# Kernel optimization log

Hardware: AMD Instinct MI355X
Metric: run time of the kernel (lower is better)

## Reference

```python
import jax, jax.numpy as jnp
import numpy as np

B, S, D, H = 4, 2048, 1024, 16
DK = D // H
THETA = 10000.0


def setup_inputs() -> dict:
    key = jax.random.key(0)
    ks = jax.random.split(key, 5)
    std = (1.0 / D) ** 0.5
    return {
        "x": jax.random.normal(ks[0], (B, S, D), dtype=jnp.float32),
        "q_proj": jax.random.normal(ks[1], (D, D), dtype=jnp.float32) * std,
        "k_proj": jax.random.normal(ks[2], (D, D), dtype=jnp.float32) * std,
        "v_proj": jax.random.normal(ks[3], (D, D), dtype=jnp.float32) * std,
        "o_proj": jax.random.normal(ks[4], (D, D), dtype=jnp.float32) * std,
        "token_positions": jnp.broadcast_to(jnp.arange(S, dtype=jnp.int32), (B, S)),
    }


def _apply_rope(t, cos, sin):
    # t: (B,H,S,DK); cos/sin: (B,1,S,DK//2). Interleaved even/odd rotation.
    even = t[..., 0::2]
    odd = t[..., 1::2]
    r_even = even * cos - odd * sin
    r_odd = even * sin + odd * cos
    return jnp.stack([r_even, r_odd], axis=-1).reshape(t.shape)


def reference(x, q_proj, k_proj, v_proj, o_proj, token_positions):
    b, s, d = x.shape
    # QKV projections: weights stored (out, in) -> x @ W^T
    q = (x @ q_proj.T).reshape(b, s, H, DK).transpose(0, 2, 1, 3)  # (B,H,S,DK)
    k = (x @ k_proj.T).reshape(b, s, H, DK).transpose(0, 2, 1, 3)
    v = (x @ v_proj.T).reshape(b, s, H, DK).transpose(0, 2, 1, 3)

    # RoPE angles from token positions
    inv_freq = 1.0 / (THETA ** (jnp.arange(0, DK, 2, dtype=jnp.float32) / DK))  # (DK/2,)
    ang = token_positions.astype(jnp.float32)[..., None] * inv_freq  # (B,S,DK/2)
    cos = jnp.cos(ang)[:, None, :, :]  # (B,1,S,DK/2)
    sin = jnp.sin(ang)[:, None, :, :]
    q = _apply_rope(q, cos, sin)
    k = _apply_rope(k, cos, sin)

    # Full causal attention with explicit score matrix (faithful to source)
    scores = jnp.einsum("bhqd,bhkd->bhqk", q, k) / (DK ** 0.5)
    causal = jnp.tril(jnp.ones((s, s), dtype=bool))
    scores = jnp.where(causal, scores, -jnp.inf)
    attn = jax.nn.softmax(scores, axis=-1)
    out = jnp.einsum("bhqk,bhkd->bhqd", attn, v)  # (B,H,S,DK)
    out = out.transpose(0, 2, 1, 3).reshape(b, s, d)  # (B,S,D)
    # o_proj stored (d_out, d_model): out @ o_proj^T
    return out @ o_proj.T
```

## Files before the change

### kernel.cpp

```cpp
#include <hip/hip_runtime.h>
#include <hip/hip_bf16.h>

using bf16x8 = __attribute__((ext_vector_type(8))) short;
using f32x4  = __attribute__((ext_vector_type(4))) float;

#define MFMA_BF16(a, b, c) __builtin_amdgcn_mfma_f32_16x16x32_bf16((a), (b), (c), 0, 0, 0)

__device__ __forceinline__ unsigned short f2bf(float x) {
  union { float f; unsigned int u; } v; v.f = x;
  unsigned int r = v.u + 0x7fffu + ((v.u >> 16) & 1u);
  return (unsigned short)(r >> 16);
}

__device__ __forceinline__ unsigned int cvtpk(float a, float b) {
  __hip_bfloat162 h = __float22bfloat162_rn(make_float2(a, b));
  unsigned int u; __builtin_memcpy(&u, &h, 4); return u;
}

__device__ __forceinline__ unsigned int pack_trunc(float a, float b) {
  unsigned int ua, ub;
  __builtin_memcpy(&ua, &a, 4);
  __builtin_memcpy(&ub, &b, 4);
  return (ua >> 16) | (ub & 0xFFFF0000u);
}

__device__ __forceinline__ float fast_exp2(float x) {
#if __has_builtin(__builtin_amdgcn_exp2f)
  return __builtin_amdgcn_exp2f(x);
#else
  return exp2f(x);
#endif
}

__device__ __forceinline__ void gload16(const void* g, void* l) {
  __builtin_amdgcn_global_load_lds(
      (const __attribute__((address_space(1))) unsigned int*)g,
      (__attribute__((address_space(3))) unsigned int*)l, 16, 0, 0);
}

__device__ __forceinline__ void wait_and_barrier() {
  asm volatile("s_waitcnt vmcnt(0)" ::: "memory");
  __builtin_amdgcn_sched_barrier(0);
  __builtin_amdgcn_s_barrier();
  __builtin_amdgcn_sched_barrier(0);
}

__global__ __launch_bounds__(256) void cvt_all(const float* __restrict__ x,
                                               const float* __restrict__ qw,
                                               const float* __restrict__ kw,
                                               const float* __restrict__ vw,
                                               const float* __restrict__ ow,
                                               unsigned short* __restrict__ out) {
  const int bid = blockIdx.x;
  int seg, loc;
  if (bid < 8192) { seg = 0; loc = bid; }
  else { seg = 1 + ((bid - 8192) >> 10); loc = (bid - 8192) & 1023; }
  const float* srcs[5] = {x, qw, kw, vw, ow};
  const float* in = srcs[seg];
  const size_t obase = (seg == 0) ? 0 : ((size_t)8192 + (size_t)(seg - 1) * 1024) * 1024;
  const int i = loc * 1024 + threadIdx.x * 4;
  float4 f = *(const float4*)(in + i);
  ushort4 o;
  o.x = f2bf(f.x); o.y = f2bf(f.y); o.z = f2bf(f.z); o.w = f2bf(f.w);
  *(ushort4*)(out + obase + i) = o;
}

__global__ __launch_bounds__(256) void rope_tab_k(const int* __restrict__ pos,
                                                  float2* __restrict__ tab) {
  const int row = blockIdx.x * 8 + (threadIdx.x >> 5);
  const int i = threadIdx.x & 31;
  const float p = (float)pos[row];
  const float invf = exp2f((float)(2 * i) * (-13.287712379549609f / 64.0f));
  float sn, cs;
  sincosf(p * invf, &sn, &cs);
  tab[(size_t)row * 32 + i] = make_float2(cs, sn);
}

template <int MODE>
__global__ __launch_bounds__(256) void gemm_bt(const unsigned short* __restrict__ A,
                                               const unsigned short* __restrict__ Bw,
                                               void* __restrict__ outp,
                                               const float2* __restrict__ tab,
                                               float oscale) {
  constexpr int K = 1024;
  __shared__ __align__(16) unsigned short smem[12288];
  const int tid  = threadIdx.x;
  const int lane = tid & 63, wave = tid >> 6;
  const int wr = wave >> 1, wc = wave & 1;
  const int bid = blockIdx.x + (blockIdx.y << 3);
  const int xcd = bid & 7;
  const int t6  = bid >> 3;
  const int bn0 = (t6 & 7) * 128;
  const int bm0 = (((t6 >> 3) << 3) + xcd) * 64;
  const int lrow = lane & 15, hi = lane >> 4, lko = hi * 8;
  const int srow = tid >> 2, scol = (tid & 3) * 8;
  const unsigned short* gA = A + (size_t)(bm0 + srow) * K + scol;
  const unsigned short* gB = Bw + (size_t)(bn0 + srow) * K + scol;
  const f32x4 z = {0.f, 0.f, 0.f, 0.f};
  f32x4 acc[2][4];
#pragma unroll
  for (int i = 0; i < 2; ++i)
#pragma unroll
    for (int j = 0; j < 4; ++j) acc[i][j] = z;

  auto stage = [&](int k0, int c) {
    char* base = (char*)smem + c * 12288;
    gload16(gA + k0, base + wave * 1024);
    gload16(gB + k0, base + 4096 + wave * 1024);
    gload16(gB + k0 + (size_t)64 * K, base + 8192 + wave * 1024);
  };

  stage(0, 0);
  int cur = 0;
#pragma unroll 1
  for (int k0 = 0; k0 < K; k0 += 32) {
    wait_and_barrier();
    if (k0 + 32 < K) stage(k0 + 32, cur ^ 1);
    const int ub = cur * 6144;
    bf16x8 af[2], bfr[4];
#pragma unroll
    for (int mi = 0; mi < 2; ++mi)
      af[mi] = *(const bf16x8*)&smem[ub + (wr * 32 + mi * 16 + lrow) * 32 + lko];
#pragma unroll
    for (int ni = 0; ni < 4; ++ni)
      bfr[ni] = *(const bf16x8*)&smem[ub + 2048 + (wc * 64 + ni * 16 + lrow) * 32 + lko];
#pragma unroll
    for (int mi = 0; mi < 2; ++mi)
#pragma unroll
      for (int ni = 0; ni < 4; ++ni)
        acc[mi][ni] = MFMA_BF16(af[mi], bfr[ni], acc[mi][ni]);
    cur ^= 1;
  }

  if (MODE == 2) {
#pragma unroll
    for (int mi = 0; mi < 2; ++mi)
#pragma unroll
      for (int r = 0; r < 4; ++r) {
        const int row = bm0 + wr * 32 + mi * 16 + hi * 4 + r;
#pragma unroll
        for (int ni = 0; ni < 4; ++ni) {
          const int col = bn0 + wc * 64 + ni * 16 + lrow;
          ((float*)outp)[(size_t)row * 1024 + col] = acc[mi][ni][r];
        }
      }
    return;
  }

  const int h0 = bn0 >> 6;
  const int bb = bm0 >> 11, s0 = bm0 & 2047;
  unsigned short* dst = (unsigned short*)outp;
  __syncthreads();
  if (MODE == 0) {
#pragma unroll
    for (int mi = 0; mi < 2; ++mi)
#pragma unroll
      for (int ni = 0; ni < 4; ++ni) {
        const int col = wc * 64 + ni * 16 + lrow;
        const int d = col & 63;
#pragma unroll
        for (int r = 0; r < 4; ++r) {
          const int row = wr * 32 + mi * 16 + hi * 4 + r;
          const float2 t = tab[(size_t)(bm0 + row) * 32 + (d >> 1)];
          const float v = acc[mi][ni][r];
          const float other = __shfl_xor(v, 1);
          const float rv = (d & 1) ? (other * t.y + v * t.x) : (v * t.x - other * t.y);
          smem[row * 136 + col] = f2bf(rv * oscale);
        }
      }
    __syncthreads();
#pragma unroll
    for (int it = 0; it < 4; ++it) {
      const int c = it * 256 + tid;
      const int hl = c >> 9, rem = c & 511;
      const int sl = rem >> 3, ch = (rem & 7) * 8;
      const bf16x8 val = *(const bf16x8*)&smem[sl * 136 + hl * 64 + ch];
      *(bf16x8*)&dst[((size_t)(bb * 16 + h0 + hl) * 2048 + s0 + sl) * 64 + ch] = val;
    }
  } else {
#pragma unroll
    for (int mi = 0; mi < 2; ++mi)
#pragma unroll
      for (int ni = 0; ni < 4; ++ni) {
        const int col = wc * 64 + ni * 16 + lrow;
        ushort4 pk;
        pk.x = f2bf(acc[mi][ni][0]); pk.y = f2bf(acc[mi][ni][1]);
        pk.z = f2bf(acc[mi][ni][2]); pk.w = f2bf(acc[mi][ni][3]);
        *(ushort4*)&smem[col * 72 + wr * 32 + mi * 16 + hi * 4] = pk;
      }
    __syncthreads();
#pragma unroll
    for (int it = 0; it < 4; ++it) {
      const int c = it * 256 + tid;
      const int cl = c >> 3, sc = (c & 7) * 8;
      const bf16x8 val = *(const bf16x8*)&smem[cl * 72 + sc];
      *(bf16x8*)&dst[((size_t)(bb * 16 + h0 + (cl >> 6)) * 64 + (cl & 63)) * 2048 + s0 + sc] = val;
    }
  }
}

__global__ __launch_bounds__(256) void attn_fwd(const unsigned short* __restrict__ Q,
                                                const unsigned short* __restrict__ Kk,
                                                const unsigned short* __restrict__ Vt,
                                                unsigned short* __restrict__ O) {
  __shared__ __align__(16) unsigned short Ks[8192];
  __shared__ __align__(16) unsigned short Vs[8192];
  __shared__ __align__(16) unsigned short Plds[4][16][64];
  const int p = blockIdx.x;
  const int L = (p & 7) * 64 + (p >> 3);
  const int bh = L >> 3, pr = L & 7;
  const int tid = threadIdx.x;
  const int lane = tid & 63, wave = tid >> 6;
  const int lrow = lane & 15, hi = lane >> 4;
  const int l7 = lrow & 7;
  const unsigned short* Qb = Q + (size_t)bh * 2048 * 64;
  const unsigned short* Kb = Kk + (size_t)bh * 2048 * 64;
  const unsigned short* Vb = Vt + (size_t)bh * 64 * 2048;
  const int rK   = tid >> 3;
  const int colK = ((tid & 7) ^ ((tid >> 3) & 7)) * 8;
  const int rV   = tid >> 4;
  const int colV = ((tid & 8) | ((tid & 7) ^ ((tid >> 4) & 7))) * 8;
  const int b = bh >> 4, h = bh & 15;
  const f32x4 z = {0.f, 0.f, 0.f, 0.f};
  const short one = (short)0x3F80;
  const bf16x8 ones = {one, one, one, one, one, one, one, one};
  const int qrl = wave * 16 + lrow;

  auto stage128 = [&](int kv0) {
#pragma unroll
    for (int pass = 0; pass < 4; ++pass)
      gload16(Kb + (size_t)(kv0 + rK + 32 * pass) * 64 + colK,
              (char*)Ks + pass * 4096 + wave * 1024);
#pragma unroll
    for (int pass = 0; pass < 4; ++pass)
      gload16(Vb + (size_t)(rV + 16 * pass) * 2048 + kv0 + colV,
              (char*)Vs + pass * 4096 + wave * 1024);
  };

  for (int half = 0; half < 2; ++half) {
    const int qb = half ? (15 - pr) : pr;
    const int qga = qb * 128 + qrl;
    const int qgb = qga + 64;
    const bf16x8 qfa0 = *(const bf16x8*)(Qb + (size_t)qga * 64 + hi * 8);
    const bf16x8 qfa1 = *(const bf16x8*)(Qb + (size_t)qga * 64 + 32 + hi * 8);
    const bf16x8 qfb0 = *(const bf16x8*)(Qb + (size_t)qgb * 64 + hi * 8);
    const bf16x8 qfb1 = *(const bf16x8*)(Qb + (size_t)qgb * 64 + 32 + hi * 8);
    f32x4 acca[4] = {z, z, z, z}, accb[4] = {z, z, z, z};
    f32x4 acc_la = z, acc_lb = z;

    auto sm_pv = [&](f32x4* st, const bf16x8* vf, f32x4* acc, f32x4& acc_l,
                     bool dg) {
      if (dg) {
#pragma unroll
        for (int n = 0; n < 4; ++n)
#pragma unroll
          for (int r = 0; r < 4; ++r)
            if (n * 16 + hi * 4 + r > qrl) st[n][r] = -1e30f;
      }
      float pe[16];
#pragma unroll
      for (int n = 0; n < 4; ++n)
#pragma unroll
        for (int r = 0; r < 4; ++r) pe[n * 4 + r] = fast_exp2(st[n][r]);
#pragma unroll
      for (int n = 0; n < 4; ++n) {
        uint2 pk;
        pk.x = pack_trunc(pe[n * 4 + 0], pe[n * 4 + 1]);
        pk.y = pack_trunc(pe[n * 4 + 2], pe[n * 4 + 3]);
        const int eo = ((((n * 2 + (hi >> 1)) ^ l7) << 3) | ((hi & 1) << 2));
        *(uint2*)&Plds[wave][lrow][eo] = pk;
      }
      const bf16x8 pf0 = *(const bf16x8*)&Plds[wave][lrow][(hi ^ l7) << 3];
      const bf16x8 pf1 = *(const bf16x8*)&Plds[wave][lrow][((4 + hi) ^ l7) << 3];
      acc_l = MFMA_BF16(ones, pf0, acc_l);
      acc_l = MFMA_BF16(ones, pf1, acc_l);
#pragma unroll
      for (int dt = 0; dt < 4; ++dt) {
        acc[dt] = MFMA_BF16(vf[dt * 2], pf0, acc[dt]);
        acc[dt] = MFMA_BF16(vf[dt * 2 + 1], pf1, acc[dt]);
      }
    };

    auto process_half = [&](const char* Kbase, const char* Vbase,
                            bool doA, bool dgA, bool dgB) {
      bf16x8 kf[8];
#pragma unroll
      for (int n = 0; n < 4; ++n) {
        const int rk = n * 16 + lrow;
        kf[n * 2]     = *(const bf16x8*)(Kbase + rk * 128 + ((hi ^ l7) * 16));
        kf[n * 2 + 1] = *(const bf16x8*)(Kbase + rk * 128 + (((4 + hi) ^ l7) * 16));
      }
      f32x4 sta[4], stb[4];
      __builtin_amdgcn_s_setprio(1);
      if (doA) {
#pragma unroll
        for (int n = 0; n < 4; ++n) {
          sta[n] = MFMA_BF16(kf[n * 2], qfa0, z);
          sta[n] = MFMA_BF16(kf[n * 2 + 1], qfa1, sta[n]);
        }
      }
#pragma unroll
      for (int n = 0; n < 4; ++n) {
        stb[n] = MFMA_BF16(kf[n * 2], qfb0, z);
        stb[n] = MFMA_BF16(kf[n * 2 + 1], qfb1, stb[n]);
      }
      __builtin_amdgcn_s_setprio(0);
      bf16x8 vf[8];
#pragma unroll
      for (int dt = 0; dt < 4; ++dt) {
        const int rv = dt * 16 + lrow;
        vf[dt * 2]     = *(const bf16x8*)(Vbase + rv * 256 + ((hi ^ l7) * 16));
        vf[dt * 2 + 1] = *(const bf16x8*)(Vbase + rv * 256 + (((4 + hi) ^ l7) * 16));
      }
      if (doA) sm_pv(sta, vf, acca, acc_la, dgA);
      sm_pv(stb, vf, accb, acc_lb, dgB);
    };

#pragma unroll 1
    for (int f = 0; f <= qb; ++f) {
      __syncthreads();
      stage128(f * 128);
      __syncthreads();
      const bool dg = (f == qb);
      process_half((char*)Ks, (char*)Vs, true, dg, false);
      process_half((char*)Ks + 8192, (char*)Vs + 128, !dg, false, dg);
    }

    const float inva = 1.0f / acc_la[0];
    const float invb = 1.0f / acc_lb[0];
#pragma unroll
    for (int dt = 0; dt < 4; ++dt) {
      uint2 ov;
      ov.x = cvtpk(acca[dt][0] * inva, acca[dt][1] * inva);
      ov.y = cvtpk(acca[dt][2] * inva, acca[dt][3] * inva);
      *(uint2*)&O[((size_t)b * 2048 + qga) * 1024 + h * 64 + dt * 16 + hi * 4] = ov;
      uint2 ow2;
      ow2.x = cvtpk(accb[dt][0] * invb, accb[dt][1] * invb);
      ow2.y = cvtpk(accb[dt][2] * invb, accb[dt][3] * invb);
      *(uint2*)&O[((size_t)b * 2048 + qgb) * 1024 + h * 64 + dt * 16 + hi * 4] = ow2;
    }
  }
}

extern "C" void kernel_launch(void* const* d_in, const int* in_sizes, int n_in,
                              void* d_out, int out_size, void* d_ws, size_t ws_size,
                              hipStream_t stream) {
  const float* x  = (const float*)d_in[0];
  const float* qw = (const float*)d_in[1];
  const float* kw = (const float*)d_in[2];
  const float* vw = (const float*)d_in[3];
  const float* ow = (const float*)d_in[4];
  const int* pos  = (const int*)d_in[5];
  float* out = (float*)d_out;

  unsigned short* xb  = (unsigned short*)d_ws;
  unsigned short* qwb = xb  + (size_t)8192 * 1024;
  unsigned short* kwb = qwb + (size_t)1024 * 1024;
  unsigned short* vwb = kwb + (size_t)1024 * 1024;
  unsigned short* owb = vwb + (size_t)1024 * 1024;
  unsigned short* Qr  = owb + (size_t)1024 * 1024;
  unsigned short* Kr  = Qr  + (size_t)8192 * 1024;
  unsigned short* Vtr = Kr  + (size_t)8192 * 1024;
  unsigned short* AO  = Vtr + (size_t)8192 * 1024;
  float2* tab = (float2*)(AO + (size_t)8192 * 1024);

  cvt_all<<<12288, 256, 0, stream>>>(x, qw, kw, vw, ow, xb);
  rope_tab_k<<<1024, 256, 0, stream>>>(pos, tab);

  constexpr float SCALE = 0.18033688011112042f;
  dim3 gg(8, 128);
  gemm_bt<0><<<gg, 256, 0, stream>>>(xb, qwb, Qr,  tab, SCALE);
  gemm_bt<0><<<gg, 256, 0, stream>>>(xb, kwb, Kr,  tab, 1.0f);
  gemm_bt<1><<<gg, 256, 0, stream>>>(xb, vwb, Vtr, nullptr, 1.0f);
  attn_fwd<<<512, 256, 0, stream>>>(Qr, Kr, Vtr, AO);
  gemm_bt<2><<<gg, 256, 0, stream>>>(AO, owb, out, nullptr, 1.0f);
}
```

Measured before the change: 177.9 us.

## Use 128x128 GEMM tiles, merge QKV launches, fuse rope table into conversion

Enlarges the projection GEMM block tile from 64x128 to 128x128, giving each wave a 64x64 sub-tile. This raises MFMA work per LDS load and halves the grid. LDS reads get an XOR swizzle to avoid bank conflicts. The three Q/K/V GEMMs run as one launch using blockIdx.z, and the RoPE table computation is folded into the fp32-to-bf16 conversion kernel, which now converts 8 elements per thread. Launch count drops, at the cost of more accumulator registers, which may lower occupancy, and fewer blocks per GPU.

```diff
diff --git a/kernel.cpp b/kernel.cpp
--- a/kernel.cpp
+++ b/kernel.cpp
@@ -50,64 +50,75 @@
                                                const float* __restrict__ kw,
                                                const float* __restrict__ vw,
                                                const float* __restrict__ ow,
-                                               unsigned short* __restrict__ out) {
+                                               unsigned short* __restrict__ out,
+                                               const int* __restrict__ pos,
+                                               float2* __restrict__ tab) {
   const int bid = blockIdx.x;
+  if (bid >= 6144) {
+    const int row = (bid - 6144) * 8 + (threadIdx.x >> 5);
+    const int i = threadIdx.x & 31;
+    const float p = (float)pos[row];
+    const float invf = exp2f((float)(2 * i) * (-13.287712379549609f / 64.0f));
+    float sn, cs;
+    sincosf(p * invf, &sn, &cs);
+    tab[(size_t)row * 32 + i] = make_float2(cs, sn);
+    return;
+  }
   int seg, loc;
-  if (bid < 8192) { seg = 0; loc = bid; }
-  else { seg = 1 + ((bid - 8192) >> 10); loc = (bid - 8192) & 1023; }
+  if (bid < 4096) { seg = 0; loc = bid; }
+  else { seg = 1 + ((bid - 4096) >> 9); loc = (bid - 4096) & 511; }
   const float* srcs[5] = {x, qw, kw, vw, ow};
   const float* in = srcs[seg];
   const size_t obase = (seg == 0) ? 0 : ((size_t)8192 + (size_t)(seg - 1) * 1024) * 1024;
-  const int i = loc * 1024 + threadIdx.x * 4;
-  float4 f = *(const float4*)(in + i);
-  ushort4 o;
-  o.x = f2bf(f.x); o.y = f2bf(f.y); o.z = f2bf(f.z); o.w = f2bf(f.w);
-  *(ushort4*)(out + obase + i) = o;
-}
-
-__global__ __launch_bounds__(256) void rope_tab_k(const int* __restrict__ pos,
-                                                  float2* __restrict__ tab) {
-  const int row = blockIdx.x * 8 + (threadIdx.x >> 5);
-  const int i = threadIdx.x & 31;
-  const float p = (float)pos[row];
-  const float invf = exp2f((float)(2 * i) * (-13.287712379549609f / 64.0f));
-  float sn, cs;
-  sincosf(p * invf, &sn, &cs);
-  tab[(size_t)row * 32 + i] = make_float2(cs, sn);
+  const int i = loc * 2048 + threadIdx.x * 8;
+  float4 f0 = *(const float4*)(in + i);
+  float4 f1 = *(const float4*)(in + i + 4);
+  bf16x8 o;
+  o[0] = (short)f2bf(f0.x); o[1] = (short)f2bf(f0.y);
+  o[2] = (short)f2bf(f0.z); o[3] = (short)f2bf(f0.w);
+  o[4] = (short)f2bf(f1.x); o[5] = (short)f2bf(f1.y);
+  o[6] = (short)f2bf(f1.z); o[7] = (short)f2bf(f1.w);
+  *(bf16x8*)(out + obase + i) = o;
 }
 
 template <int MODE>
-__global__ __launch_bounds__(256) void gemm_bt(const unsigned short* __restrict__ A,
-                                               const unsigned short* __restrict__ Bw,
+__global__ __launch_bounds__(256) void gemm128(const unsigned short* __restrict__ A,
+                                               const unsigned short* __restrict__ W,
                                                void* __restrict__ outp,
-                                               const float2* __restrict__ tab,
-                                               float oscale) {
+                                               const float2* __restrict__ tab) {
   constexpr int K = 1024;
-  __shared__ __align__(16) unsigned short smem[12288];
+  constexpr float SCALE = 0.18033688011112042f;
+  constexpr int SMEM_ELEMS = (MODE == 0) ? 17408 : 16384;
+  __shared__ __align__(16) unsigned short smem[SMEM_ELEMS];
   const int tid  = threadIdx.x;
   const int lane = tid & 63, wave = tid >> 6;
   const int wr = wave >> 1, wc = wave & 1;
+  const int z = (MODE == 0) ? blockIdx.z : 0;
+  const unsigned short* Bw = W + (size_t)z * 1048576;
   const int bid = blockIdx.x + (blockIdx.y << 3);
   const int xcd = bid & 7;
   const int t6  = bid >> 3;
   const int bn0 = (t6 & 7) * 128;
-  const int bm0 = (((t6 >> 3) << 3) + xcd) * 64;
-  const int lrow = lane & 15, hi = lane >> 4, lko = hi * 8;
-  const int srow = tid >> 2, scol = (tid & 3) * 8;
+  const int bm0 = (((t6 >> 3) << 3) + xcd) * 128;
+  const int lrow = lane & 15, hi = lane >> 4;
+  const int srow = tid >> 2;
+  const int scol = ((tid & 3) ^ (srow & 3) ^ ((srow >> 2) & 3)) * 8;
   const unsigned short* gA = A + (size_t)(bm0 + srow) * K + scol;
   const unsigned short* gB = Bw + (size_t)(bn0 + srow) * K + scol;
-  const f32x4 z = {0.f, 0.f, 0.f, 0.f};
-  f32x4 acc[2][4];
-#pragma unroll
-  for (int i = 0; i < 2; ++i)
-#pragma unroll
-    for (int j = 0; j < 4; ++j) acc[i][j] = z;
+  const int sw2 = (lrow & 3) ^ ((lrow >> 2) & 3);
+  const f32x4 z4 = {0.f, 0.f, 0.f, 0.f};
+  f32x4 acc[4][4];
+#pragma unroll
+  for (int i = 0; i < 4; ++i)
+#pragma unroll
+    for (int j = 0; j < 4; ++j) acc[i][j] = z4;
 
   auto stage = [&](int k0, int c) {
-    char* base = (char*)smem + c * 12288;
-    gload16(gA + k0, base + wave * 1024);
-    gload16(gB + k0, base + 4096 + wave * 1024);
-    gload16(gB + k0 + (size_t)64 * K, base + 8192 + wave * 1024);
+    char* base = (char*)smem + c * 16384;
+    gload16(gA + k0,                 base +         wave * 1024);
+    gload16(gA + k0 + (size_t)64 * K, base + 4096 + wave * 1024);
+    gload16(gB + k0,                 base + 8192 + wave * 1024);
+    gload16(gB + k0 + (size_t)64 * K, base + 12288 + wave * 1024);
   };
 
   stage(0, 0);
@@ -116,16 +127,16 @@
   for (int k0 = 0; k0 < K; k0 += 32) {
     wait_and_barrier();
     if (k0 + 32 < K) stage(k0 + 32, cur ^ 1);
-    const int ub = cur * 6144;
-    bf16x8 af[2], bfr[4];
-#pragma unroll
-    for (int mi = 0; mi < 2; ++mi)
-      af[mi] = *(const bf16x8*)&smem[ub + (wr * 32 + mi * 16 + lrow) * 32 + lko];
+    const char* ub = (const char*)smem + cur * 16384;
+    bf16x8 af[4], bfr[4];
+#pragma unroll
+    for (int mi = 0; mi < 4; ++mi)
+      af[mi] = *(const bf16x8*)(ub + (wr * 64 + mi * 16 + lrow) * 64 + ((hi ^ sw2) * 16));
 #pragma unroll
     for (int ni = 0; ni < 4; ++ni)
-      bfr[ni] = *(const bf16x8*)&smem[ub + 2048 + (wc * 64 + ni * 16 + lrow) * 32 + lko];
-#pragma unroll
-    for (int mi = 0; mi < 2; ++mi)
+      bfr[ni] = *(const bf16x8*)(ub + 8192 + (wc * 64 + ni * 16 + lrow) * 64 + ((hi ^ sw2) * 16));
+#pragma unroll
+    for (int mi = 0; mi < 4; ++mi)
 #pragma unroll
       for (int ni = 0; ni < 4; ++ni)
         acc[mi][ni] = MFMA_BF16(af[mi], bfr[ni], acc[mi][ni]);
@@ -134,10 +145,10 @@
 
   if (MODE == 2) {
 #pragma unroll
-    for (int mi = 0; mi < 2; ++mi)
+    for (int mi = 0; mi < 4; ++mi)
 #pragma unroll
       for (int r = 0; r < 4; ++r) {
-        const int row = bm0 + wr * 32 + mi * 16 + hi * 4 + r;
+        const int row = bm0 + wr * 64 + mi * 16 + hi * 4 + r;
 #pragma unroll
         for (int ni = 0; ni < 4; ++ni) {
           const int col = bn0 + wc * 64 + ni * 16 + lrow;
@@ -149,18 +160,21 @@
 
   const int h0 = bn0 >> 6;
   const int bb = bm0 >> 11, s0 = bm0 & 2047;
-  unsigned short* dst = (unsigned short*)outp;
+  unsigned short* Qr = (unsigned short*)outp;
+  unsigned short* dst = (z == 0) ? Qr : (z == 1 ? Qr + (size_t)8388608
+                                                : Qr + (size_t)16777216);
+  const float oscale = (z == 0) ? SCALE : 1.0f;
   __syncthreads();
-  if (MODE == 0) {
-#pragma unroll
-    for (int mi = 0; mi < 2; ++mi)
+  if (z < 2) {
+#pragma unroll
+    for (int mi = 0; mi < 4; ++mi)
 #pragma unroll
       for (int ni = 0; ni < 4; ++ni) {
         const int col = wc * 64 + ni * 16 + lrow;
         const int d = col & 63;
 #pragma unroll
         for (int r = 0; r < 4; ++r) {
-          const int row = wr * 32 + mi * 16 + hi * 4 + r;
+          const int row = wr * 64 + mi * 16 + hi * 4 + r;
           const float2 t = tab[(size_t)(bm0 + row) * 32 + (d >> 1)];
           const float v = acc[mi][ni][r];
           const float other = __shfl_xor(v, 1);
@@ -170,30 +184,30 @@
       }
     __syncthreads();
 #pragma unroll
-    for (int it = 0; it < 4; ++it) {
+    for (int it = 0; it < 8; ++it) {
       const int c = it * 256 + tid;
-      const int hl = c >> 9, rem = c & 511;
+      const int hl = c >> 10, rem = c & 1023;
       const int sl = rem >> 3, ch = (rem & 7) * 8;
       const bf16x8 val = *(const bf16x8*)&smem[sl * 136 + hl * 64 + ch];
       *(bf16x8*)&dst[((size_t)(bb * 16 + h0 + hl) * 2048 + s0 + sl) * 64 + ch] = val;
     }
   } else {
 #pragma unroll
-    for (int mi = 0; mi < 2; ++mi)
+    for (int mi = 0; mi < 4; ++mi)
 #pragma unroll
       for (int ni = 0; ni < 4; ++ni) {
         const int col = wc * 64 + ni * 16 + lrow;
         ushort4 pk;
         pk.x = f2bf(acc[mi][ni][0]); pk.y = f2bf(acc[mi][ni][1]);
         pk.z = f2bf(acc[mi][ni][2]); pk.w = f2bf(acc[mi][ni][3]);
-        *(ushort4*)&smem[col * 72 + wr * 32 + mi * 16 + hi * 4] = pk;
+        *(ushort4*)&smem[col * 136 + wr * 64 + mi * 16 + hi * 4] = pk;
       }
     __syncthreads();
 #pragma unroll
-    for (int it = 0; it < 4; ++it) {
+    for (int it = 0; it < 8; ++it) {
       const int c = it * 256 + tid;
-      const int cl = c >> 3, sc = (c & 7) * 8;
-      const bf16x8 val = *(const bf16x8*)&smem[cl * 72 + sc];
+      const int cl = c >> 4, sc = (c & 15) * 8;
+      const bf16x8 val = *(const bf16x8*)&smem[cl * 136 + sc];
       *(bf16x8*)&dst[((size_t)(bb * 16 + h0 + (cl >> 6)) * 64 + (cl & 63)) * 2048 + s0 + sc] = val;
     }
   }
@@ -355,23 +369,19 @@
 
   unsigned short* xb  = (unsigned short*)d_ws;
   unsigned short* qwb = xb  + (size_t)8192 * 1024;
-  unsigned short* kwb = qwb + (size_t)1024 * 1024;
-  unsigned short* vwb = kwb + (size_t)1024 * 1024;
-  unsigned short* owb = vwb + (size_t)1024 * 1024;
+  unsigned short* owb = qwb + (size_t)3 * 1024 * 1024;
   unsigned short* Qr  = owb + (size_t)1024 * 1024;
   unsigned short* Kr  = Qr  + (size_t)8192 * 1024;
   unsigned short* Vtr = Kr  + (size_t)8192 * 1024;
   unsigned short* AO  = Vtr + (size_t)8192 * 1024;
   float2* tab = (float2*)(AO + (size_t)8192 * 1024);
-
-  cvt_all<<<12288, 256, 0, stream>>>(x, qw, kw, vw, ow, xb);
-  rope_tab_k<<<1024, 256, 0, stream>>>(pos, tab);
-
-  constexpr float SCALE = 0.18033688011112042f;
-  dim3 gg(8, 128);
-  gemm_bt<0><<<gg, 256, 0, stream>>>(xb, qwb, Qr,  tab, SCALE);
-  gemm_bt<0><<<gg, 256, 0, stream>>>(xb, kwb, Kr,  tab, 1.0f);
-  gemm_bt<1><<<gg, 256, 0, stream>>>(xb, vwb, Vtr, nullptr, 1.0f);
+  (void)Kr; (void)Vtr;
+
+  cvt_all<<<7168, 256, 0, stream>>>(x, qw, kw, vw, ow, xb, pos, tab);
+
+  dim3 gqkv(8, 64, 3);
+  gemm128<0><<<gqkv, 256, 0, stream>>>(xb, qwb, Qr, tab);
   attn_fwd<<<512, 256, 0, stream>>>(Qr, Kr, Vtr, AO);
-  gemm_bt<2><<<gg, 256, 0, stream>>>(AO, owb, out, nullptr, 1.0f);
-}
+  dim3 go(8, 64);
+  gemm128<2><<<go, 256, 0, stream>>>(AO, owb, out, nullptr);
+}
```

After: 157.4 us. 1.13x faster.
